# Kernel optimization log

Measured on AMD Instinct MI355X. Metric: run time of the kernel, lower is better.

## Reference

```python
import jax, jax.numpy as jnp
import numpy as np
from jax import lax

SOFTMAX_SCALE = 10.0  # module hardcodes self.softmax_scale = 10
NORM_EPS = 1e-4


def extract_patches(x, ksize, stride, pad=1):
    """torch F.unfold(..., padding=1) -> [B, L, C, ksize, ksize], L = oh*ow row-major."""
    B, C, H, W = x.shape
    xp = jnp.pad(x, ((0, 0), (0, 0), (pad, pad), (pad, pad)))
    oh = (H + 2 * pad - ksize) // stride + 1
    ow = (W + 2 * pad - ksize) // stride + 1
    cols = jnp.stack(
        [xp[:, :, i:i + (oh - 1) * stride + 1:stride, j:j + (ow - 1) * stride + 1:stride]
         for i in range(ksize) for j in range(ksize)], axis=2)  # [B, C, k*k, oh, ow]
    cols = cols.reshape(B, C, ksize, ksize, oh * ow)
    return cols.transpose(0, 4, 1, 2, 3)  # [B, L, C, k, k]


def contextual_attention(fg, bg, mask, rate, stride, ksize):
    B, C, H, W = fg.shape
    # raw background patches at full resolution, used for reconstruction
    bg_cols = extract_patches(bg, 2 * rate, rate * stride)  # [B, L, C, 2r, 2r]
    if rate != 1:  # nearest-neighbor downsample by rate (F.upsample scale=1/rate)
        fg = fg[:, :, ::rate, ::rate]
        bg = bg[:, :, ::rate, ::rate]
        mask = mask[:, :, ::rate, ::rate]
    # patch validity: 1 where the mask patch is entirely zero (known background)
    mask_cols = extract_patches(mask, ksize, stride)  # [B, L, 1, k, k]
    mm = (jnp.sum(mask_cols, axis=(2, 3, 4)) == 0.0).astype(fg.dtype)  # [B, L]
    # L2-normalized background kernels
    kern = extract_patches(bg, ksize, stride)  # [B, L, C, k, k]
    norm = jnp.sqrt(jnp.sum(kern * kern, axis=(2, 3, 4), keepdims=True))
    kern = kern / jnp.maximum(norm, NORM_EPS)
    # per-sample correlation (batched im2col GEMM instead of per-sample conv2d)
    Bh, Bw = fg.shape[2], fg.shape[3]
    fgp = extract_patches(fg, ksize, stride)  # [B, P, C, k, k], P = Bh*Bw
    scores = jnp.einsum('bpckm,blckm->blp', fgp, kern).reshape(B, -1, Bh, Bw)
    # masked, scaled softmax over patch dimension
    mm4 = mm[:, :, None, None]
    attn = jax.nn.softmax(SOFTMAX_SCALE * (scores * mm4), axis=1) * mm4  # [B, L, Bh, Bw]
    # reconstruct: per-sample conv_transpose2d(attn, bg_cols, stride=rate, padding=1) / 4
    K = 2 * rate

    def recon_one(a, kcols):  # a: [L, Bh, Bw], kcols: [L, C, K, K]
        w = jnp.flip(kcols, axis=(2, 3)).transpose(1, 0, 2, 3)  # [C, L, K, K]
        y = lax.conv_general_dilated(
            a[None], w, window_strides=(1, 1),
            padding=[(K - 2, K - 2), (K - 2, K - 2)],  # K-1-pad, pad=1
            lhs_dilation=(rate, rate),
            dimension_numbers=('NCHW', 'OIHW', 'NCHW'))
        return y[0]

    out = jax.vmap(recon_one)(attn, bg_cols) / 4.0  # [B, C, H, W]
    return out


def setup_inputs() -> dict:
    key = jax.random.key(0)
    k1, k2, k3 = jax.random.split(key, 3)
    B, C, H, W = 8, 16, 128, 128
    foreground = jax.random.normal(k1, (B, C, H, W), dtype=jnp.float32)
    background = jax.random.normal(k2, (B, C, H, W), dtype=jnp.float32)
    mask = jax.random.randint(k3, (B, 1, H, W), 0, 2).astype(jnp.float32)
    return {"foreground": foreground, "background": background, "mask": mask,
            "rate": 2, "stride": 1, "ksize": 3}


def reference(foreground, background, mask, rate, stride, ksize):
    return contextual_attention(foreground, background, mask, rate, stride, ksize)
```

## Files before the change

### kernel.cpp

```cpp
#include <hip/hip_runtime.h>
#include <hip/hip_bf16.h>
#include <hip/hip_fp16.h>

#define BB 8
#define CC 16
#define HH 128
#define WW 128
#define HD 64
#define WD 64
#define LP 4096
#define K1 144
#define KP 160
#define N2 256
#define E60 8.75651076269652e-27f

typedef __attribute__((ext_vector_type(8))) short bf16x8;
typedef __attribute__((ext_vector_type(8))) _Float16 f16x8;
typedef __attribute__((ext_vector_type(4))) float f32x4;

__device__ __forceinline__ unsigned short pack_rne(float x) {
    unsigned int u = __float_as_uint(x);
    return (unsigned short)((u + 0x7FFFu + ((u >> 16) & 1u)) >> 16);
}
__device__ __forceinline__ float bf2f(unsigned short u) {
    return __uint_as_float(((unsigned int)u) << 16);
}
__device__ __forceinline__ unsigned short f2h(float x) {
    return __half_as_ushort(__float2half(x));
}
__device__ __forceinline__ float ld_in(const void* p, long idx, int bf) {
    if (bf) return bf2f(((const unsigned short*)p)[idx]);
    return ((const float*)p)[idx];
}
__device__ __forceinline__ void gl_lds16(const void* g, void* l) {
    __builtin_amdgcn_global_load_lds(
        (const __attribute__((address_space(1))) unsigned int*)g,
        (__attribute__((address_space(3))) unsigned int*)l,
        16, 0, 0);
}

__global__ void detect_kernel(const unsigned int* __restrict__ w,
                              int* __restrict__ flag, int* __restrict__ cnt) {
    int lane = threadIdx.x;
    if (lane < BB) cnt[lane] = 0;
    int c = 0;
    for (int i = lane; i < 256; i += 64) {
        unsigned int e = (w[i] >> 7) & 0xFF;
        if (e >= 100 && e <= 140) c++;
    }
#pragma unroll
    for (int s = 1; s < 64; s <<= 1) c += __shfl_xor(c, s);
    if (lane == 0) *flag = (c >= 192) ? 1 : 0;
}

__global__ __launch_bounds__(256) void prep_kernel(
    const void* __restrict__ fg, const void* __restrict__ bg,
    const void* __restrict__ mask, const int* __restrict__ flagp,
    unsigned short* __restrict__ Fp, int* __restrict__ cnt,
    unsigned short* __restrict__ Kc, unsigned short* __restrict__ Vc)
{
    int bf = *flagp;
    int wave = threadIdx.x >> 6, lane = threadIdx.x & 63;
    int bl = blockIdx.x * 4 + wave;
    int b = bl >> 12, l = bl & 4095;
    int py = l >> 6, px = l & 63;

    float fgv[3], bgv[3];
    float ss = 0.f;
#pragma unroll
    for (int j = 0; j < 3; j++) {
        int e = lane + 64 * j;
        fgv[j] = 0.f; bgv[j] = 0.f;
        if (e < K1) {
            int c = e / 9;
            int r9 = e - c * 9;
            int ky = r9 / 3, kx = r9 - ky * 3;
            int yy = py + ky - 1, xx = px + kx - 1;
            if (yy >= 0 && yy < HD && xx >= 0 && xx < WD) {
                long base = ((long)(b * CC + c) * HH + 2 * yy) * WW + 2 * xx;
                fgv[j] = ld_in(fg, base, bf);
                bgv[j] = ld_in(bg, base, bf);
            }
        }
        ss += bgv[j] * bgv[j];
    }
#pragma unroll
    for (int s = 1; s < 64; s <<= 1) ss += __shfl_xor(ss, s);
    float rn = 1.0f / fmaxf(sqrtf(ss), 1e-4f);

    float mv = 0.f;
    if (lane < 9) {
        int ky = lane / 3, kx = lane - ky * 3;
        int yy = py + ky - 1, xx = px + kx - 1;
        if (yy >= 0 && yy < HD && xx >= 0 && xx < WD)
            mv = ld_in(mask, ((long)b * HH + 2 * yy) * WW + 2 * xx, bf);
    }
#pragma unroll
    for (int s = 1; s < 16; s <<= 1) mv += __shfl_xor(mv, s);
    float mvall = __shfl(mv, 0);

    long base = (long)bl * KP;
#pragma unroll
    for (int j = 0; j < 3; j++) {
        int e = lane + 64 * j;
        if (e < KP) Fp[base + e] = f2h(fgv[j]);
    }

    if (mvall == 0.0f) {
        int j0;
        if (lane == 0) j0 = atomicAdd(&cnt[b], 1);
        int j = __shfl(j0, 0);
        size_t kb = ((size_t)b * LP + j) * KP;
#pragma unroll
        for (int q = 0; q < 3; q++) {
            int e = lane + 64 * q;
            if (e < KP) Kc[kb + e] = f2h(bgv[q] * rn);
        }
        unsigned short* vcb = Vc + (size_t)b * N2 * LP + j;
#pragma unroll
        for (int q = 0; q < 4; q++) {
            int e = lane + 64 * q;
            int c = e >> 4, dy = (e >> 2) & 3, dx = e & 3;
            int Y = 2 * py + dy - 1, X = 2 * px + dx - 1;
            float v = 0.f;
            if (Y >= 0 && Y < HH && X >= 0 && X < WW)
                v = ld_in(bg, ((long)(b * CC + c) * HH + Y) * WW + X, bf);
            vcb[(size_t)e * LP] = pack_rne(v);
        }
    }
}

__global__ __launch_bounds__(256) void zpad_kernel(
    const int* __restrict__ cnt, unsigned short* __restrict__ Vc)
{
    int b = blockIdx.x;
    int n = cnt[b];
    int npad = (n + 31) & ~31;
    unsigned short* row = Vc + ((size_t)b * N2 + threadIdx.x) * LP;
    for (int j = n; j < npad; j++) row[j] = 0;
}

__global__ __launch_bounds__(256, 2) void flash_kernel(
    const unsigned short* __restrict__ Fp, const unsigned short* __restrict__ Kc,
    const unsigned short* __restrict__ Vc,
    const int* __restrict__ cnt,
    unsigned short* __restrict__ U)
{
    __shared__ char S_lds[2][26624];
    __shared__ unsigned short P_lds[4][2][16][40];

    int t = threadIdx.x;
    int wave = t >> 6, lane = t & 63;
    int l15 = lane & 15, lq = lane >> 4;

    int b = blockIdx.y;
    int pw = blockIdx.x * 128 + wave * 32;

    const unsigned short* Fp_b = Fp + (size_t)b * LP * KP;
    const unsigned short* Kc_b = Kc + (size_t)b * LP * KP;
    const unsigned short* Vc_b = Vc + (size_t)b * N2 * LP;

    int n = cnt[b];
    int nch = (n + 31) >> 5;

    unsigned int vdiff = (unsigned int)(Vc_b - Kc_b);
    unsigned int soff[7], smul[7];
#pragma unroll
    for (int j = 0; j < 7; j++) {
        int i = wave + 4 * j;
        int d = i * 1024 + lane * 16;
        if (i < 10) {
            int kc = d >> 11, slot = (d >> 9) & 3, row = (d >> 4) & 31;
            soff[j] = row * KP + kc * 32 + slot * 8;
            smul[j] = KP;
        } else {
            int d2 = d - 10240;
            int slot = d2 >> 12, c = (d2 >> 4) & 255;
            soff[j] = vdiff + c * LP + slot * 8;
            smul[j] = 1;
        }
    }
    int ncall = (wave < 2) ? 7 : 6;
    int dustart = wave * 1024;

    f16x8 fA[5], fB[5];
    {
        size_t fbA = (size_t)(pw + l15) * KP + lq * 8;
        size_t fbB = (size_t)(pw + 16 + l15) * KP + lq * 8;
#pragma unroll
        for (int kc = 0; kc < 5; kc++) {
            fA[kc] = *(const f16x8*)&Fp_b[fbA + kc * 32];
            fB[kc] = *(const f16x8*)&Fp_b[fbB + kc * 32];
        }
    }

    f32x4 zero4 = {0.f, 0.f, 0.f, 0.f};
    f32x4 accA[16], accB[16];
#pragma unroll
    for (int nn = 0; nn < 16; nn++) { accA[nn] = zero4; accB[nn] = zero4; }
    float dA[4] = {0.f, 0.f, 0.f, 0.f};
    float dB[4] = {0.f, 0.f, 0.f, 0.f};

    if (nch > 0) {
#pragma unroll
        for (int j = 0; j < 7; j++)
            if (j < ncall)
                gl_lds16(Kc_b + soff[j], &S_lds[0][dustart + j * 4096]);
    }

    for (int ch = 0; ch < nch; ch++) {
        int cur = ch & 1;
        int l0 = ch * 32;
        __syncthreads();

        float mmh0 = (l0 + l15 < n) ? 1.f : 0.f;
        float mmh1 = (l0 + 16 + l15 < n) ? 1.f : 0.f;

        if (ch + 1 < nch) {
            size_t ln = (size_t)(l0 + 32);
#pragma unroll
            for (int j = 0; j < 7; j++)
                if (j < ncall)
                    gl_lds16(Kc_b + soff[j] + ln * smul[j], &S_lds[cur ^ 1][dustart + j * 4096]);
        }

        float eA[2][4], eB[2][4];
#pragma unroll
        for (int h = 0; h < 2; h++) {
            const char* kb = &S_lds[cur][lq * 512 + (h * 16 + l15) * 16];
            f32x4 sA = zero4, sB = zero4;
#pragma unroll
            for (int kc = 0; kc < 5; kc++) {
                f16x8 kv = *(const f16x8*)(kb + kc * 2048);
                sA = __builtin_amdgcn_mfma_f32_16x16x32_f16(fA[kc], kv, sA, 0, 0, 0);
                sB = __builtin_amdgcn_mfma_f32_16x16x32_f16(fB[kc], kv, sB, 0, 0, 0);
            }
            float mmh = h ? mmh1 : mmh0;
#pragma unroll
            for (int r = 0; r < 4; r++) {
                float zA = (mmh > 0.f) ? 10.f * sA[r] : 0.f;
                float zB = (mmh > 0.f) ? 10.f * sB[r] : 0.f;
                float ea = __expf(zA - 60.f);
                float eb = __expf(zB - 60.f);
                dA[r] += ea; dB[r] += eb;
                eA[h][r] = ea * mmh; eB[h][r] = eb * mmh;
            }
        }

#pragma unroll
        for (int h = 0; h < 2; h++)
#pragma unroll
            for (int r = 0; r < 4; r++) {
                P_lds[wave][0][lq * 4 + r][h * 16 + l15] = pack_rne(eA[h][r]);
                P_lds[wave][1][lq * 4 + r][h * 16 + l15] = pack_rne(eB[h][r]);
            }
        bf16x8 pa0 = *(const bf16x8*)&P_lds[wave][0][l15][lq * 8];
        bf16x8 pa1 = *(const bf16x8*)&P_lds[wave][1][l15][lq * 8];

        const char* Vcp = &S_lds[cur][10240 + lq * 4096];
#pragma unroll
        for (int g = 0; g < 4; g++) {
            bf16x8 vb[4];
#pragma unroll
            for (int nn = 0; nn < 4; nn++)
                vb[nn] = *(const bf16x8*)(Vcp + (g * 64 + nn * 16 + l15) * 16);
#pragma unroll
            for (int nn = 0; nn < 4; nn++) {
                accA[g * 4 + nn] = __builtin_amdgcn_mfma_f32_16x16x32_bf16(pa0, vb[nn], accA[g * 4 + nn], 0, 0, 0);
                accB[g * 4 + nn] = __builtin_amdgcn_mfma_f32_16x16x32_bf16(pa1, vb[nn], accB[g * 4 + nn], 0, 0, 0);
            }
        }
    }

#pragma unroll
    for (int s = 1; s < 16; s <<= 1)
#pragma unroll
        for (int r = 0; r < 4; r++) {
            dA[r] += __shfl_xor(dA[r], s);
            dB[r] += __shfl_xor(dB[r], s);
        }
    float corr = (float)(LP - nch * 32) * E60;
    float diA[4], diB[4];
#pragma unroll
    for (int r = 0; r < 4; r++) {
        diA[r] = 1.0f / (dA[r] + corr);
        diB[r] = 1.0f / (dB[r] + corr);
    }

    unsigned short* Uo = U + (size_t)b * LP * N2;
#pragma unroll
    for (int g = 0; g < 4; g++)
#pragma unroll
        for (int nn = 0; nn < 4; nn++) {
            int col = g * 64 + nn * 16 + l15;
#pragma unroll
            for (int r = 0; r < 4; r++) {
                Uo[(size_t)(pw + lq * 4 + r) * N2 + col] = pack_rne(accA[g * 4 + nn][r] * diA[r]);
                Uo[(size_t)(pw + 16 + lq * 4 + r) * N2 + col] = pack_rne(accB[g * 4 + nn][r] * diB[r]);
            }
        }
}

__global__ __launch_bounds__(256) void gather_kernel(
    const unsigned short* __restrict__ U, float* __restrict__ out)
{
    int idx = blockIdx.x * 256 + threadIdx.x;
    int ox = idx & 127;
    int t1 = idx >> 7;
    int oy = t1 & 127;
    int t2 = t1 >> 7;
    int c = t2 & 15;
    int b = t2 >> 4;

    float sum = 0.f;
    int d0y = (oy + 1) & 1, d0x = (ox + 1) & 1;
#pragma unroll
    for (int iy = 0; iy < 2; iy++) {
        int dy = d0y + 2 * iy;
        int y = (oy + 1 - dy) >> 1;
        if (y < 0 || y > 63) continue;
#pragma unroll
        for (int ix = 0; ix < 2; ix++) {
            int dx = d0x + 2 * ix;
            int x = (ox + 1 - dx) >> 1;
            if (x < 0 || x > 63) continue;
            sum += bf2f(U[((long)b * LP + y * 64 + x) * N2 + c * 16 + dy * 4 + dx]);
        }
    }
    out[idx] = sum * 0.25f;
}

extern "C" void kernel_launch(void* const* d_in, const int* in_sizes, int n_in,
                              void* d_out, int out_size, void* d_ws, size_t ws_size,
                              hipStream_t stream)
{
    const void* fg   = d_in[0];
    const void* bg   = d_in[1];
    const void* mask = d_in[2];
    float* out = (float*)d_out;

    char* w = (char*)d_ws;
    size_t o = 0;
    int*            flag = (int*)(w + o);            o += 16;
    int*            cnt  = (int*)(w + o);            o += 64;
    unsigned short* Fp   = (unsigned short*)(w + o); o += (size_t)BB * LP * KP * 2;
    unsigned short* Kc   = (unsigned short*)(w + o); o += (size_t)BB * LP * KP * 2;
    unsigned short* Vc   = (unsigned short*)(w + o); o += (size_t)BB * N2 * LP * 2;
    unsigned short* U    = (unsigned short*)(w + o); o += (size_t)BB * LP * N2 * 2;

    detect_kernel<<<1, 64, 0, stream>>>((const unsigned int*)fg, flag, cnt);
    prep_kernel<<<BB * LP / 4, 256, 0, stream>>>(fg, bg, mask, flag, Fp, cnt, Kc, Vc);
    zpad_kernel<<<BB, 256, 0, stream>>>(cnt, Vc);

    flash_kernel<<<dim3(LP / 128, BB), 256, 0, stream>>>(Fp, Kc, Vc, cnt, U);

    gather_kernel<<<(BB * CC * HH * WW) / 256, 256, 0, stream>>>(U, out);
}
```

Before: 129.7 us.

## Stage prep input rows in shared memory and process a full patch row per block

The prep kernel now assigns one block per downsampled row and batch. It loads the three needed input rows of fg, bg and mask into shared memory once, then builds the im2col patches, norms and mask validity from shared memory instead of issuing redundant strided global loads per patch. The Fp tile is assembled in LDS and written out with coalesced 16-byte stores. Valid patches are compacted through a shared list before Kc/Vc are emitted. In exchange the grid shrinks to 512 blocks, and each block uses a large amount of shared memory, which may limit occupancy.

Measured after the change: 120.3 us. 1.08x faster.

```diff
diff --git a/kernel.cpp b/kernel.cpp
--- a/kernel.cpp
+++ b/kernel.cpp
@@ -59,69 +59,121 @@
     unsigned short* __restrict__ Fp, int* __restrict__ cnt,
     unsigned short* __restrict__ Kc, unsigned short* __restrict__ Vc)
 {
+    __shared__ float sFg[3][16][64];
+    __shared__ float sBg[3][16][64];
+    __shared__ float sMask[3][64];
+    __shared__ __align__(16) unsigned short pFp[64][160];
+    __shared__ float red[64][4];
+    __shared__ float rn_sh[64];
+    __shared__ int selPx[64];
+    __shared__ int nsel;
+
     int bf = *flagp;
-    int wave = threadIdx.x >> 6, lane = threadIdx.x & 63;
-    int bl = blockIdx.x * 4 + wave;
-    int b = bl >> 12, l = bl & 4095;
-    int py = l >> 6, px = l & 63;
-
-    float fgv[3], bgv[3];
+    int t = threadIdx.x;
+    int py = blockIdx.x;
+    int b  = blockIdx.y;
+
+    if (t == 0) nsel = 0;
+
+#pragma unroll
+    for (int i = 0; i < 12; i++) {
+        int q = t + 256 * i;
+        int rr = q >> 10;
+        int rem = q & 1023;
+        int c = rem >> 6, xe = rem & 63;
+        int Y = 2 * py + 2 * rr - 2;
+        float fv = 0.f, bv = 0.f;
+        if (Y >= 0 && Y < HH) {
+            long gidx = ((long)(b * CC + c) * HH + Y) * WW + 2 * xe;
+            fv = ld_in(fg, gidx, bf);
+            bv = ld_in(bg, gidx, bf);
+        }
+        sFg[rr][c][xe] = fv;
+        sBg[rr][c][xe] = bv;
+    }
+    if (t < 192) {
+        int rr = t >> 6, xe = t & 63;
+        int Y = 2 * py + 2 * rr - 2;
+        float mv = 0.f;
+        if (Y >= 0 && Y < HH)
+            mv = ld_in(mask, ((long)b * HH + Y) * WW + 2 * xe, bf);
+        sMask[rr][xe] = mv;
+    }
+    __syncthreads();
+
+    int px = t & 63, g = t >> 6;
     float ss = 0.f;
-#pragma unroll
-    for (int j = 0; j < 3; j++) {
-        int e = lane + 64 * j;
-        fgv[j] = 0.f; bgv[j] = 0.f;
-        if (e < K1) {
-            int c = e / 9;
-            int r9 = e - c * 9;
-            int ky = r9 / 3, kx = r9 - ky * 3;
-            int yy = py + ky - 1, xx = px + kx - 1;
-            if (yy >= 0 && yy < HD && xx >= 0 && xx < WD) {
-                long base = ((long)(b * CC + c) * HH + 2 * yy) * WW + 2 * xx;
-                fgv[j] = ld_in(fg, base, bf);
-                bgv[j] = ld_in(bg, base, bf);
-            }
-        }
-        ss += bgv[j] * bgv[j];
-    }
-#pragma unroll
-    for (int s = 1; s < 64; s <<= 1) ss += __shfl_xor(ss, s);
-    float rn = 1.0f / fmaxf(sqrtf(ss), 1e-4f);
-
-    float mv = 0.f;
-    if (lane < 9) {
-        int ky = lane / 3, kx = lane - ky * 3;
-        int yy = py + ky - 1, xx = px + kx - 1;
-        if (yy >= 0 && yy < HD && xx >= 0 && xx < WD)
-            mv = ld_in(mask, ((long)b * HH + 2 * yy) * WW + 2 * xx, bf);
-    }
-#pragma unroll
-    for (int s = 1; s < 16; s <<= 1) mv += __shfl_xor(mv, s);
-    float mvall = __shfl(mv, 0);
-
-    long base = (long)bl * KP;
-#pragma unroll
-    for (int j = 0; j < 3; j++) {
-        int e = lane + 64 * j;
-        if (e < KP) Fp[base + e] = f2h(fgv[j]);
-    }
-
-    if (mvall == 0.0f) {
-        int j0;
+    for (int c = 4 * g; c < 4 * g + 4; c++) {
+#pragma unroll
+        for (int ky = 0; ky < 3; ky++)
+#pragma unroll
+            for (int kx = 0; kx < 3; kx++) {
+                int xi = px + kx - 1;
+                float fv = 0.f, bv = 0.f;
+                if (xi >= 0 && xi < 64) { fv = sFg[ky][c][xi]; bv = sBg[ky][c][xi]; }
+                ss += bv * bv;
+                pFp[px][c * 9 + ky * 3 + kx] = f2h(fv);
+            }
+    }
+    if (g == 0) {
+#pragma unroll
+        for (int e = K1; e < KP; e++) pFp[px][e] = 0;
+    }
+    red[px][g] = ss;
+    __syncthreads();
+
+    if (g == 0) {
+        float S = red[px][0] + red[px][1] + red[px][2] + red[px][3];
+        rn_sh[px] = 1.0f / fmaxf(sqrtf(S), 1e-4f);
+    } else if (g == 1) {
+        float mv = 0.f;
+#pragma unroll
+        for (int ky = 0; ky < 3; ky++)
+#pragma unroll
+            for (int kx = 0; kx < 3; kx++) {
+                int xi = px + kx - 1;
+                if (xi >= 0 && xi < 64) mv += sMask[ky][xi];
+            }
+        if (mv == 0.0f) selPx[atomicAdd(&nsel, 1)] = px;
+    }
+    __syncthreads();
+
+    {
+        const uint4* src = (const uint4*)&pFp[0][0];
+        uint4* dst = (uint4*)(Fp + ((size_t)b * LP + (size_t)py * 64) * KP);
+#pragma unroll
+        for (int i = 0; i < 5; i++) dst[t + 256 * i] = src[t + 256 * i];
+    }
+
+    int lane = t & 63;
+    for (int i = g; i < nsel; i += 4) {
+        int p2 = selPx[i];
+        int j0 = 0;
         if (lane == 0) j0 = atomicAdd(&cnt[b], 1);
         int j = __shfl(j0, 0);
+        float rn = rn_sh[p2];
         size_t kb = ((size_t)b * LP + j) * KP;
 #pragma unroll
         for (int q = 0; q < 3; q++) {
             int e = lane + 64 * q;
-            if (e < KP) Kc[kb + e] = f2h(bgv[q] * rn);
+            if (e < KP) {
+                float bv = 0.f;
+                if (e < K1) {
+                    int c = e / 9;
+                    int r9 = e - c * 9;
+                    int ky = r9 / 3, kx = r9 - ky * 3;
+                    int xi = p2 + kx - 1;
+                    if (xi >= 0 && xi < 64) bv = sBg[ky][c][xi];
+                }
+                Kc[kb + e] = f2h(bv * rn);
+            }
         }
         unsigned short* vcb = Vc + (size_t)b * N2 * LP + j;
 #pragma unroll
         for (int q = 0; q < 4; q++) {
             int e = lane + 64 * q;
             int c = e >> 4, dy = (e >> 2) & 3, dx = e & 3;
-            int Y = 2 * py + dy - 1, X = 2 * px + dx - 1;
+            int Y = 2 * py + dy - 1, X = 2 * p2 + dx - 1;
             float v = 0.f;
             if (Y >= 0 && Y < HH && X >= 0 && X < WW)
                 v = ld_in(bg, ((long)(b * CC + c) * HH + Y) * WW + X, bf);
@@ -349,7 +401,7 @@
     unsigned short* U    = (unsigned short*)(w + o); o += (size_t)BB * LP * N2 * 2;
 
     detect_kernel<<<1, 64, 0, stream>>>((const unsigned int*)fg, flag, cnt);
-    prep_kernel<<<BB * LP / 4, 256, 0, stream>>>(fg, bg, mask, flag, Fp, cnt, Kc, Vc);
+    prep_kernel<<<dim3(64, BB), 256, 0, stream>>>(fg, bg, mask, flag, Fp, cnt, Kc, Vc);
     zpad_kernel<<<BB, 256, 0, stream>>>(cnt, Vc);
 
     flash_kernel<<<dim3(LP / 128, BB), 256, 0, stream>>>(Fp, Kc, Vc, cnt, U);
```
